# Performance work log

Measured on AMD Instinct MI355X. Metric: run time of the kernel, lower is better.

The kernel has to match this reference:

```python
import jax, jax.numpy as jnp
import numpy as np

B, N, K, H, NF = 4, 4096, 20, 64, 128
EPS = 1e-5  # BatchNorm eps (inference mode)


def _knn_idx(x):
    # x: (B, C, N); returns indices of K nearest neighbors (incl. self), (B, N, K)
    xx = jnp.sum(x * x, axis=1)                      # (B, N)
    inner = jnp.einsum('bcn,bcm->bnm', x, x)         # (B, N, N)
    neg_dist = 2.0 * inner - xx[:, :, None] - xx[:, None, :]
    return jax.lax.top_k(neg_dist, K)[1]


def _graph_feat(x, first):
    # x: (B, C, N) -> edge features (B, C', N, K)
    idx = _knn_idx(x)                                # (B, N, K)
    xt = jnp.transpose(x, (0, 2, 1))                 # (B, N, C)
    nb = jax.vmap(lambda f, i: f[i])(xt, idx)        # (B, N, K, C)
    nb = jnp.transpose(nb, (0, 3, 1, 2))             # (B, C, N, K)
    c = jnp.broadcast_to(x[:, :, :, None], nb.shape)
    parts = [nb - c]
    if first:  # cross term only in first block (3-dim coords)
        parts.append(jnp.cross(c, nb, axis=1))
    parts.append(c)
    return jnp.concatenate(parts, axis=1)


def _conv_bn_lrelu(x, W, g, b, m, v):
    # 1x1 conv (no bias) + BatchNorm (inference) + LeakyReLU(0.2)
    y = jnp.einsum('oc,bc...->bo...', W, x)
    scale = g / jnp.sqrt(v + EPS)
    sh = (1, -1) + (1,) * (y.ndim - 2)
    y = y * scale.reshape(sh) + (b - m * scale).reshape(sh)
    return jnp.where(y >= 0, y, 0.2 * y)


def _forward(x, layers, We, Wh, bh):
    x = jnp.transpose(x, (0, 2, 1))                  # (B, 3, N)
    outs = []
    for li in range(4):
        gf = _graph_feat(x, li == 0)                 # (B, cin, N, K)
        y = _conv_bn_lrelu(gf, *layers[li])          # (B, cout, N, K)
        x = jnp.max(y, axis=-1)                      # max-pool over neighbors
        outs.append(x)
    cat = jnp.concatenate(outs, axis=1)              # (B, 512, N)
    y = _conv_bn_lrelu(cat, *layers[4])              # final Conv1d block
    y = jnp.max(y, axis=-1)                          # global max over points
    emb = y @ We.T                                   # Linear(512, NF, bias=False)
    return emb @ Wh.T + bh                           # embedding_head


def setup_inputs() -> dict:
    key = jax.random.key(0)
    ks = jax.random.split(key, 40)

    def nrm(k, shape, s=0.1):
        return jax.random.normal(k, shape, jnp.float32) * s

    inp = {'x': jax.random.normal(ks[0], (B, N, 3), jnp.float32)}
    dims = [(9, H), (2 * H, H), (2 * H, 2 * H), (4 * H, 4 * H), (8 * H, 8 * H)]
    i = 1
    for li, (cin, cout) in enumerate(dims):
        inp['W%d' % li] = nrm(ks[i], (cout, cin)); i += 1
        inp['g%d' % li] = 1.0 + nrm(ks[i], (cout,), 0.05); i += 1
        inp['b%d' % li] = nrm(ks[i], (cout,), 0.05); i += 1
        inp['m%d' % li] = nrm(ks[i], (cout,), 0.05); i += 1
        inp['v%d' % li] = 1.0 + jax.random.uniform(ks[i], (cout,)) * 0.1; i += 1
    inp['We'] = nrm(ks[i], (NF, 8 * H)); i += 1
    inp['Wh'] = nrm(ks[i], (NF, NF)); i += 1
    inp['bh'] = nrm(ks[i], (NF,))
    return inp


def reference(x, W0, g0, b0, m0, v0, W1, g1, b1, m1, v1, W2, g2, b2, m2, v2,
              W3, g3, b3, m3, v3, W4, g4, b4, m4, v4, We, Wh, bh):
    layers = [(W0, g0, b0, m0, v0), (W1, g1, b1, m1, v1), (W2, g2, b2, m2, v2),
              (W3, g3, b3, m3, v3), (W4, g4, b4, m4, v4)]
    return _forward(x, layers, We, Wh, bh)
```

## Files before the change

### kernel.cpp

```cpp
#include <hip/hip_runtime.h>
#include <cfloat>

#define N_PTS 4096
#define NB    4
#define KNN   20
#define EPSB  1e-5f
#define NSL   4

typedef short s8v __attribute__((ext_vector_type(8)));
typedef float f4v __attribute__((ext_vector_type(4)));

__device__ __forceinline__ void bf16split(float x, unsigned short* h, unsigned short* l)
{
    unsigned u = __builtin_bit_cast(unsigned, x);
    unsigned hb = (u + 0x7fffu + ((u >> 16) & 1u)) >> 16;
    float hf = __builtin_bit_cast(float, hb << 16);
    float res = x - hf;
    unsigned u2 = __builtin_bit_cast(unsigned, res);
    unsigned lb = (u2 + 0x7fffu + ((u2 >> 16) & 1u)) >> 16;
    *h = (unsigned short)hb;
    *l = (unsigned short)lb;
}

__device__ __forceinline__ unsigned packkey(float d, int lc)
{
    d = fmaxf(d, 0.f);
    unsigned u = __builtin_bit_cast(unsigned, d);
    return (u & 0xFFFFFF00u) | (unsigned)lc;
}

__device__ __forceinline__ void insert20k(unsigned key, unsigned (&k20)[KNN])
{
#pragma unroll
    for (int j = 0; j < KNN; j++) {
        unsigned old = k20[j];
        unsigned lo = old < key ? old : key;
        key = old < key ? key : old;
        k20[j] = lo;
    }
}

__device__ __forceinline__ void gl2lds16(const void* g, void* l)
{
    __builtin_amdgcn_global_load_lds(
        (const __attribute__((address_space(1))) unsigned int*)g,
        (__attribute__((address_space(3))) unsigned int*)l,
        16, 0, 0);
}

__device__ __forceinline__ int swz(int g)
{
    return g ^ (((g >> 3) ^ (g >> 6)) & 7);
}

__global__ __launch_bounds__(256)
void to_bf16_pm(const float* __restrict__ F, long bsF, int ldF, int C, int KDP,
                unsigned short* __restrict__ Ghi, unsigned short* __restrict__ Glo)
{
    int b = blockIdx.y;
    int n = blockIdx.x * 64 + (threadIdx.x & 63);
    int kq = threadIdx.x >> 6;
    const float* Fr = F + (long)b * bsF + (long)n * ldF;
    for (int k0 = kq * 8; k0 < KDP; k0 += 32) {
        s8v hv, lv;
#pragma unroll
        for (int i = 0; i < 8; i++) {
            int k = k0 + i;
            float x = (k < C) ? Fr[k] : 0.f;
            unsigned short h, l;
            bf16split(x, &h, &l);
            hv[i] = (short)h;
            lv[i] = (short)l;
        }
        long o = ((long)b * N_PTS + n) * KDP + k0;
        *(s8v*)&Ghi[o] = hv;
        *(s8v*)&Glo[o] = lv;
    }
}

__global__ void sqnorm_pm(const float* __restrict__ F, float* __restrict__ xx,
                          int C, int ldF, long bsF)
{
    int b = blockIdx.y;
    int i = blockIdx.x * 256 + threadIdx.x;
    const float* r = F + (long)b * bsF + (long)i * ldF;
    float s = 0.f;
    for (int c = 0; c < C; c++) s = fmaf(r[c], r[c], s);
    xx[(long)b * N_PTS + i] = s;
}

template<int KDP>
__global__ __launch_bounds__(256, 3)
void fused_knn_mfma7(const unsigned short* __restrict__ Ghi,
                     const unsigned short* __restrict__ Glo,
                     const float* __restrict__ xx,
                     float* __restrict__ knnd, int* __restrict__ knni)
{
    constexpr int KS = KDP / 32;
    constexpr int TS = 16 * KDP;
    constexpr int NCH = (TS * 2) / 16;
    __shared__ short cbuf[2][2][TS];
    __shared__ unsigned mk[4][16][4][KNN];

    int tid = threadIdx.x;
    int w = tid >> 6, L = tid & 63;
    int n = L & 15;
    int quad = L >> 4;
    int b = blockIdx.z, slice = blockIdx.y;
    int q0 = blockIdx.x * 64, qw = w * 16;
    const unsigned short* Gh = Ghi + (long)b * N_PTS * KDP;
    const unsigned short* Gl = Glo + (long)b * N_PTS * KDP;
    const float* xxb = xx + (long)b * N_PTS;

    s8v qhi[KS], qlo[KS];
    long qbase = (long)(q0 + qw + n) * KDP + quad * 8;
#pragma unroll
    for (int ks = 0; ks < KS; ks++) {
        qhi[ks] = *(const s8v*)&Gh[qbase + ks * 32];
        qlo[ks] = *(const s8v*)&Gl[qbase + ks * 32];
    }
    float xq = xxb[q0 + qw + n];

    unsigned k20[KNN];
#pragma unroll
    for (int j = 0; j < KNN; j++) k20[j] = 0xFFFFFFFFu;

    int po[KS];
#pragma unroll
    for (int ks = 0; ks < KS; ks++) {
        int gL = n * (KDP / 8) + quad + ks * 4;
        po[ks] = swz(gL) * 8;
    }
    int gsrc = swz(tid);

    int w64 = tid & 192;
    {
        long tb = (long)(slice * 1024) * KDP;
        if (tid < NCH) {
            gl2lds16((const char*)(Gh + tb) + gsrc * 16,
                     (char*)&cbuf[0][0][0] + w64 * 16);
            gl2lds16((const char*)(Gl + tb) + gsrc * 16,
                     (char*)&cbuf[0][1][0] + w64 * 16);
        }
    }
    __syncthreads();

    const float* xcp = xxb + slice * 1024 + quad * 4;

    for (int t = 0; t < 64; t++) {
        int cur = t & 1;
        if (t < 63 && tid < NCH) {
            long tb = (long)(slice * 1024 + (t + 1) * 16) * KDP;
            gl2lds16((const char*)(Gh + tb) + gsrc * 16,
                     (char*)&cbuf[cur ^ 1][0][0] + w64 * 16);
            gl2lds16((const char*)(Gl + tb) + gsrc * 16,
                     (char*)&cbuf[cur ^ 1][1][0] + w64 * 16);
        }

        const short* Ch = &cbuf[cur][0][0];
        const short* Cl = &cbuf[cur][1][0];
        f4v acc = {0.f, 0.f, 0.f, 0.f};
#pragma unroll
        for (int ks = 0; ks < KS; ks++) {
            s8v chi = *(const s8v*)&Ch[po[ks]];
            s8v clo = *(const s8v*)&Cl[po[ks]];
            acc = __builtin_amdgcn_mfma_f32_16x16x32_bf16(chi, qhi[ks], acc, 0, 0, 0);
            acc = __builtin_amdgcn_mfma_f32_16x16x32_bf16(chi, qlo[ks], acc, 0, 0, 0);
            acc = __builtin_amdgcn_mfma_f32_16x16x32_bf16(clo, qhi[ks], acc, 0, 0, 0);
        }
        float4 xc4 = *(const float4*)xcp;
        float xcv[4] = {xc4.x, xc4.y, xc4.z, xc4.w};
#pragma unroll
        for (int r = 0; r < 4; r++) {
            float d = xq + xcv[r] - 2.f * acc[r];
            insert20k(packkey(d, t * 4 + r), k20);
        }
        xcp += 16;
        __syncthreads();
    }

#pragma unroll
    for (int j = 0; j < KNN; j++) mk[w][n][quad][j] = k20[j];
    __syncthreads();
    if (L < 16) {
        int p[4] = {0, 0, 0, 0};
        long o = (((long)b * NSL + slice) * N_PTS + (q0 + qw + L)) * KNN;
#pragma unroll
        for (int j = 0; j < KNN; j++) {
            unsigned bd = 0xFFFFFF00u; int bi = 0x7fffffff; int bq = 0;
#pragma unroll
            for (int qd = 0; qd < 4; qd++) {
                unsigned kk = mk[w][L][qd][p[qd]];
                unsigned db = kk & 0xFFFFFF00u;
                int lc = (int)(kk & 0xFFu);
                int ci = slice * 1024 + (lc >> 2) * 16 + qd * 4 + (lc & 3);
                if (db < bd || (db == bd && ci < bi)) { bd = db; bi = ci; bq = qd; }
            }
            knnd[o + j] = __builtin_bit_cast(float, bd);
            knni[o + j] = bi;
            p[bq]++;
        }
    }
}

__global__ void knn_merge4(const float* __restrict__ knnd, const int* __restrict__ knni,
                           int* __restrict__ idxOut)
{
    int id = blockIdx.x * 256 + threadIdx.x;
    int b = id / N_PTS, i = id % N_PTS;
    const float* dl[NSL]; const int* il[NSL];
#pragma unroll
    for (int qt = 0; qt < NSL; qt++) {
        dl[qt] = knnd + (((long)b * NSL + qt) * N_PTS + i) * KNN;
        il[qt] = knni + (((long)b * NSL + qt) * N_PTS + i) * KNN;
    }
    int p[NSL];
#pragma unroll
    for (int qt = 0; qt < NSL; qt++) p[qt] = 0;
    int* o = idxOut + (long)id * KNN;
#pragma unroll
    for (int j = 0; j < KNN; j++) {
        float best = FLT_MAX; int bi = 0x7fffffff; int bq = 0;
#pragma unroll
        for (int qt = 0; qt < NSL; qt++) {
            float vv = (p[qt] < KNN) ? dl[qt][p[qt]] : FLT_MAX;
            int   ci = (p[qt] < KNN) ? il[qt][p[qt]] : 0x7fffffff;
            if (vv < best || (vv == best && ci < bi)) { best = vv; bi = ci; bq = qt; }
        }
        o[j] = bi;
        p[bq]++;
    }
}

template<int KDP>
__global__ __launch_bounds__(256)
void qp_mfma(const unsigned short* __restrict__ Ghi,
             const unsigned short* __restrict__ Glo,
             const unsigned short* __restrict__ Wqh, const unsigned short* __restrict__ Wql,
             const unsigned short* __restrict__ Wph, const unsigned short* __restrict__ Wpl,
             const float* __restrict__ shf,
             float* __restrict__ qv, float* __restrict__ pv, int cout)
{
    constexpr int KS = KDP / 32;
    int tid = threadIdx.x;
    int w = tid >> 6, L = tid & 63;
    int n = L & 15, quad = L >> 4;
    int b = blockIdx.z;
    int p0 = blockIdx.x * 64 + w * 16;

    s8v ah[KS], al[KS];
    long abase = ((long)b * N_PTS + p0 + n) * KDP + quad * 8;
#pragma unroll
    for (int ks = 0; ks < KS; ks++) {
        ah[ks] = *(const s8v*)&Ghi[abase + ks * 32];
        al[ks] = *(const s8v*)&Glo[abase + ks * 32];
    }

#pragma unroll
    for (int oc4 = 0; oc4 < 4; oc4++) {
        int oc = blockIdx.y * 4 + oc4;
        long wbase = (long)(oc * 16 + n) * KDP + quad * 8;
        f4v aq = {0.f, 0.f, 0.f, 0.f};
        f4v ap = {0.f, 0.f, 0.f, 0.f};
#pragma unroll
        for (int ks = 0; ks < KS; ks++) {
            s8v wh = *(const s8v*)&Wqh[wbase + ks * 32];
            s8v wl = *(const s8v*)&Wql[wbase + ks * 32];
            aq = __builtin_amdgcn_mfma_f32_16x16x32_bf16(ah[ks], wh, aq, 0, 0, 0);
            aq = __builtin_amdgcn_mfma_f32_16x16x32_bf16(ah[ks], wl, aq, 0, 0, 0);
            aq = __builtin_amdgcn_mfma_f32_16x16x32_bf16(al[ks], wh, aq, 0, 0, 0);
            s8v ph = *(const s8v*)&Wph[wbase + ks * 32];
            s8v pl = *(const s8v*)&Wpl[wbase + ks * 32];
            ap = __builtin_amdgcn_mfma_f32_16x16x32_bf16(ah[ks], ph, ap, 0, 0, 0);
            ap = __builtin_amdgcn_mfma_f32_16x16x32_bf16(ah[ks], pl, ap, 0, 0, 0);
            ap = __builtin_amdgcn_mfma_f32_16x16x32_bf16(al[ks], ph, ap, 0, 0, 0);
        }
        float sv = shf[oc * 16 + n];
#pragma unroll
        for (int r = 0; r < 4; r++) {
            long pt = p0 + quad * 4 + r;
            long o = ((long)b * N_PTS + pt) * cout + oc * 16 + n;
            qv[o] = aq[r];
            pv[o] = ap[r] + sv;
        }
    }
}

__global__ __launch_bounds__(256)
void conv4_mfma(const unsigned short* __restrict__ CTh, const unsigned short* __restrict__ CTl,
                const unsigned short* __restrict__ W4h, const unsigned short* __restrict__ W4l,
                const float* __restrict__ shf, float* __restrict__ Y)
{
    int tid = threadIdx.x;
    int w = tid >> 6, L = tid & 63;
    int n = L & 15, quad = L >> 4;
    int b = blockIdx.y;
    int p0 = blockIdx.x * 16;
    const unsigned short* cth = CTh + ((long)b * N_PTS + p0 + n) * 512 + quad * 8;
    const unsigned short* ctl = CTl + ((long)b * N_PTS + p0 + n) * 512 + quad * 8;

    f4v acc[8];
#pragma unroll
    for (int ch = 0; ch < 8; ch++) acc[ch] = {0.f, 0.f, 0.f, 0.f};

    for (int ks = 0; ks < 16; ks++) {
        s8v bh = *(const s8v*)&cth[ks * 32];
        s8v bl = *(const s8v*)&ctl[ks * 32];
#pragma unroll
        for (int ch = 0; ch < 8; ch++) {
            long o = (long)((w * 8 + ch) * 16 + n) * 512 + quad * 8 + ks * 32;
            s8v ahv = *(const s8v*)&W4h[o];
            s8v alv = *(const s8v*)&W4l[o];
            acc[ch] = __builtin_amdgcn_mfma_f32_16x16x32_bf16(ahv, bh, acc[ch], 0, 0, 0);
            acc[ch] = __builtin_amdgcn_mfma_f32_16x16x32_bf16(ahv, bl, acc[ch], 0, 0, 0);
            acc[ch] = __builtin_amdgcn_mfma_f32_16x16x32_bf16(alv, bh, acc[ch], 0, 0, 0);
        }
    }
#pragma unroll
    for (int ch = 0; ch < 8; ch++) {
#pragma unroll
        for (int r = 0; r < 4; r++) {
            int o = (w * 8 + ch) * 16 + quad * 4 + r;
            float y = acc[ch][r] + shf[o];
            y = y >= 0.f ? y : 0.2f * y;
            Y[((long)b * 512 + o) * N_PTS + p0 + n] = y;
        }
    }
}

__global__ void fold_edge_bf16(const float* __restrict__ W, const float* __restrict__ g,
                               const float* __restrict__ bb, const float* __restrict__ m,
                               const float* __restrict__ v,
                               unsigned short* __restrict__ Wqh, unsigned short* __restrict__ Wql,
                               unsigned short* __restrict__ Wph, unsigned short* __restrict__ Wpl,
                               float* __restrict__ shift, int C, int cout)
{
    int id = blockIdx.x * 256 + threadIdx.x;
    if (id < C * cout) {
        int o = id / C;
        int c = id % C;
        float sc = g[o] * rsqrtf(v[o] + EPSB);
        float wd = W[(long)o * 2 * C + c];
        float wc = W[(long)o * 2 * C + C + c];
        bf16split(sc * wd, &Wqh[id], &Wql[id]);
        bf16split(sc * (wc - wd), &Wph[id], &Wpl[id]);
    }
    if (id < cout) {
        float sc = g[id] * rsqrtf(v[id] + EPSB);
        shift[id] = bb[id] - m[id] * sc;
    }
}

__global__ void fold_plain_bf16(const float* __restrict__ W, const float* __restrict__ g,
                                const float* __restrict__ bb, const float* __restrict__ m,
                                const float* __restrict__ v,
                                unsigned short* __restrict__ W4h, unsigned short* __restrict__ W4l,
                                float* __restrict__ shift, int C, int cout)
{
    int id = blockIdx.x * 256 + threadIdx.x;
    if (id < C * cout) {
        int o = id / C;
        int c = id % C;
        float sc = g[o] * rsqrtf(v[o] + EPSB);
        bf16split(sc * W[(long)o * C + c], &W4h[id], &W4l[id]);
    }
    if (id < cout) {
        float sc = g[id] * rsqrtf(v[id] + EPSB);
        shift[id] = bb[id] - m[id] * sc;
    }
}

__global__ void gather_max_pm(const float* __restrict__ q, const float* __restrict__ p,
                              const int* __restrict__ idx, float* __restrict__ cat,
                              int cout, int c_off)
{
    int b = blockIdx.y;
    int i = blockIdx.x * 4 + threadIdx.y;
    int tx = threadIdx.x;
    const int* ip = idx + ((long)b * N_PTS + i) * KNN;
    int js[KNN];
#pragma unroll
    for (int k = 0; k < KNN; k++) js[k] = ip[k];
    const float* qb = q + (long)b * N_PTS * cout;
    const float* pb = p + ((long)b * N_PTS + i) * cout;
    float* ob = cat + ((long)b * N_PTS + i) * 512 + c_off;
    for (int o0 = 0; o0 < cout; o0 += 64) {
        int o = o0 + tx;
        float pv = pb[o];
        float mx = -FLT_MAX;
#pragma unroll
        for (int k = 0; k < KNN; k++) {
            float val = qb[(long)js[k] * cout + o] + pv;
            val = val >= 0.f ? val : 0.2f * val;
            mx = fmaxf(mx, val);
        }
        ob[o] = mx;
    }
}

__global__ void edge0_pm(const float* __restrict__ x, const int* __restrict__ idx,
                         const float* __restrict__ W0, const float* __restrict__ g0,
                         const float* __restrict__ b0, const float* __restrict__ m0,
                         const float* __restrict__ v0, float* __restrict__ cat)
{
    int b = blockIdx.y;
    int i = blockIdx.x * 4 + threadIdx.y;
    int o = threadIdx.x;
    const float* xc = x + ((long)b * N_PTS + i) * 3;
    float cx = xc[0], cy = xc[1], cz = xc[2];
    float w[9];
#pragma unroll
    for (int c = 0; c < 9; c++) w[c] = W0[o * 9 + c];
    float sc = g0[o] * rsqrtf(v0[o] + EPSB);
    float sh = b0[o] - m0[o] * sc;
    const int* ip = idx + ((long)b * N_PTS + i) * KNN;
    float mx = -FLT_MAX;
#pragma unroll
    for (int k = 0; k < KNN; k++) {
        const float* xn = x + ((long)b * N_PTS + ip[k]) * 3;
        float nx = xn[0], ny = xn[1], nz = xn[2];
        float dx = nx - cx, dy = ny - cy, dz = nz - cz;
        float crx = cy * nz - cz * ny;
        float cry = cz * nx - cx * nz;
        float crz = cx * ny - cy * nx;
        float y = w[0] * dx + w[1] * dy + w[2] * dz
                + w[3] * crx + w[4] * cry + w[5] * crz
                + w[6] * cx + w[7] * cy + w[8] * cz;
        y = y * sc + sh;
        y = y >= 0.f ? y : 0.2f * y;
        mx = fmaxf(mx, y);
    }
    cat[((long)b * N_PTS + i) * 512 + o] = mx;
}

__global__ void rowmax_kernel(const float* __restrict__ Y, float* __restrict__ ymax)
{
    __shared__ float red[256];
    int b = blockIdx.y, o = blockIdx.x, t = threadIdx.x;
    const float* yb = Y + ((long)b * 512 + o) * N_PTS;
    float mx = -FLT_MAX;
#pragma unroll
    for (int s = 0; s < N_PTS / 256; s++) mx = fmaxf(mx, yb[t + 256 * s]);
    red[t] = mx;
    __syncthreads();
    for (int off = 128; off > 0; off >>= 1) {
        if (t < off) red[t] = fmaxf(red[t], red[t + off]);
        __syncthreads();
    }
    if (t == 0) ymax[(long)b * 512 + o] = red[0];
}

__global__ void head_kernel(const float* __restrict__ ymax, const float* __restrict__ We,
                            const float* __restrict__ Wh, const float* __restrict__ bh,
                            float* __restrict__ out)
{
    __shared__ float emb[128];
    __shared__ float yv[512];
    int b = blockIdx.x, t = threadIdx.x;
    for (int s = t; s < 512; s += 128) yv[s] = ymax[(long)b * 512 + s];
    __syncthreads();
    float acc = 0.f;
    for (int c = 0; c < 512; c++) acc = fmaf(yv[c], We[(long)t * 512 + c], acc);
    emb[t] = acc;
    __syncthreads();
    float acc2 = bh[t];
    for (int ff = 0; ff < 128; ff++) acc2 = fmaf(emb[ff], Wh[(long)t * 128 + ff], acc2);
    out[(long)b * 128 + t] = acc2;
}

extern "C" void kernel_launch(void* const* d_in, const int* in_sizes, int n_in,
                              void* d_out, int out_size, void* d_ws, size_t ws_size,
                              hipStream_t stream)
{
    const float* x = (const float*)d_in[0];
    const float *W[5], *g[5], *bb[5], *m[5], *v[5];
    for (int li = 0; li < 5; li++) {
        W[li]  = (const float*)d_in[1 + li * 5 + 0];
        g[li]  = (const float*)d_in[1 + li * 5 + 1];
        bb[li] = (const float*)d_in[1 + li * 5 + 2];
        m[li]  = (const float*)d_in[1 + li * 5 + 3];
        v[li]  = (const float*)d_in[1 + li * 5 + 4];
    }
    const float* We = (const float*)d_in[26];
    const float* Wh = (const float*)d_in[27];
    const float* bh = (const float*)d_in[28];
    float* out = (float*)d_out;

    float* ws   = (float*)d_ws;
    float* cat  = ws;
    float* qbuf = cat + (long)8388608;
    float* pbuf = qbuf + (long)8388608;
    int*   idxb = (int*)(pbuf + 4194304);
    float* xx   = (float*)(idxb + 327680);
    unsigned short* Wqh = (unsigned short*)(xx + 16384);
    unsigned short* Wql = Wqh + 32768;
    unsigned short* Wph = Wql + 32768;
    unsigned short* Wpl = Wph + 32768;
    unsigned short* W4h = Wpl + 32768;
    unsigned short* W4l = W4h + 262144;
    float* shf  = (float*)(W4l + 262144);
    float* ymax = shf + 512;
    unsigned short* Ghi = (unsigned short*)qbuf;
    unsigned short* Glo = Ghi + 2097152;
    float* knnd = qbuf + 2097152;
    int*   knni = (int*)(qbuf + 2097152 + 1310720);
    float* qv   = qbuf + 2097152;
    unsigned short* CTh = (unsigned short*)qbuf;
    unsigned short* CTl = CTh + 8388608;

    sqnorm_pm<<<dim3(16, NB), dim3(256), 0, stream>>>(x, xx, 3, 3, (long)3 * N_PTS);
    to_bf16_pm<<<dim3(64, NB), dim3(256), 0, stream>>>(
        x, (long)3 * N_PTS, 3, 3, 32, Ghi, Glo);
    fused_knn_mfma7<32><<<dim3(64, NSL, NB), dim3(256), 0, stream>>>(
        Ghi, Glo, xx, knnd, knni);
    knn_merge4<<<dim3(64), dim3(256), 0, stream>>>(knnd, knni, idxb);
    edge0_pm<<<dim3(N_PTS / 4, NB), dim3(64, 4), 0, stream>>>(
        x, idxb, W[0], g[0], bb[0], m[0], v[0], cat);

    const int Cs_[3]   = {64, 64, 128};
    const int co_[3]   = {64, 128, 256};
    const int inO_[3]  = {0, 64, 128};
    const int outO_[3] = {64, 128, 256};
    for (int s = 0; s < 3; s++) {
        int C = Cs_[s], cout = co_[s];
        const float* F = cat + inO_[s];
        sqnorm_pm<<<dim3(16, NB), dim3(256), 0, stream>>>(
            F, xx, C, 512, (long)N_PTS * 512);
        to_bf16_pm<<<dim3(64, NB), dim3(256), 0, stream>>>(
            F, (long)N_PTS * 512, 512, C, C, Ghi, Glo);
        if (C == 64)
            fused_knn_mfma7<64><<<dim3(64, NSL, NB), dim3(256), 0, stream>>>(
                Ghi, Glo, xx, knnd, knni);
        else
            fused_knn_mfma7<128><<<dim3(64, NSL, NB), dim3(256), 0, stream>>>(
                Ghi, Glo, xx, knnd, knni);
        knn_merge4<<<dim3(64), dim3(256), 0, stream>>>(knnd, knni, idxb);

        int li = s + 1;
        fold_edge_bf16<<<dim3((C * cout + 255) / 256), dim3(256), 0, stream>>>(
            W[li], g[li], bb[li], m[li], v[li], Wqh, Wql, Wph, Wpl, shf, C, cout);
        if (C == 64)
            qp_mfma<64><<<dim3(64, cout / 64, NB), dim3(256), 0, stream>>>(
                Ghi, Glo, Wqh, Wql, Wph, Wpl, shf, qv, pbuf, cout);
        else
            qp_mfma<128><<<dim3(64, cout / 64, NB), dim3(256), 0, stream>>>(
                Ghi, Glo, Wqh, Wql, Wph, Wpl, shf, qv, pbuf, cout);
        gather_max_pm<<<dim3(N_PTS / 4, NB), dim3(64, 4), 0, stream>>>(
            qv, pbuf, idxb, cat, cout, outO_[s]);
    }

    fold_plain_bf16<<<dim3((512 * 512 + 255) / 256), dim3(256), 0, stream>>>(
        W[4], g[4], bb[4], m[4], v[4], W4h, W4l, shf, 512, 512);
    to_bf16_pm<<<dim3(64, NB), dim3(256), 0, stream>>>(
        cat, (long)N_PTS * 512, 512, 512, 512, CTh, CTl);
    conv4_mfma<<<dim3(N_PTS / 16, NB), dim3(256), 0, stream>>>(
        CTh, CTl, W4h, W4l, shf, cat);

    rowmax_kernel<<<dim3(512, NB), dim3(256), 0, stream>>>(cat, ymax);
    head_kernel<<<dim3(NB), dim3(128), 0, stream>>>(ymax, We, Wh, bh, out);
}
```

Baseline: 1.097 ms.

## Fuse bf16 split and squared norms into producer kernels, drop standalone conversion passes

The edge0 and gather-max kernels now emit the bf16 hi/lo split and per-point squared norm of their output directly, replacing the separate sqnorm and to_bf16 passes before each kNN stage. The final conv reads fp32 cat and splits to bf16 in-register, removing the 512-channel conversion pass and its buffer. Conv output goes to a separate buffer instead of overwriting cat. This trades extra conversion ALU work inside conv4 (repeated per block) for fewer launches and less memory traffic.

```diff
diff --git a/kernel.cpp b/kernel.cpp
--- a/kernel.cpp
+++ b/kernel.cpp
@@ -287,25 +287,33 @@
 }
 
 __global__ __launch_bounds__(256)
-void conv4_mfma(const unsigned short* __restrict__ CTh, const unsigned short* __restrict__ CTl,
-                const unsigned short* __restrict__ W4h, const unsigned short* __restrict__ W4l,
-                const float* __restrict__ shf, float* __restrict__ Y)
+void conv4f_mfma(const float* __restrict__ cat,
+                 const unsigned short* __restrict__ W4h, const unsigned short* __restrict__ W4l,
+                 const float* __restrict__ shf, float* __restrict__ Y)
 {
     int tid = threadIdx.x;
     int w = tid >> 6, L = tid & 63;
     int n = L & 15, quad = L >> 4;
     int b = blockIdx.y;
     int p0 = blockIdx.x * 16;
-    const unsigned short* cth = CTh + ((long)b * N_PTS + p0 + n) * 512 + quad * 8;
-    const unsigned short* ctl = CTl + ((long)b * N_PTS + p0 + n) * 512 + quad * 8;
+    const float* cr = cat + ((long)b * N_PTS + p0 + n) * 512 + quad * 8;
 
     f4v acc[8];
 #pragma unroll
     for (int ch = 0; ch < 8; ch++) acc[ch] = {0.f, 0.f, 0.f, 0.f};
 
     for (int ks = 0; ks < 16; ks++) {
-        s8v bh = *(const s8v*)&cth[ks * 32];
-        s8v bl = *(const s8v*)&ctl[ks * 32];
+        float4 f0 = *(const float4*)&cr[ks * 32];
+        float4 f1 = *(const float4*)&cr[ks * 32 + 4];
+        float fv[8] = {f0.x, f0.y, f0.z, f0.w, f1.x, f1.y, f1.z, f1.w};
+        s8v bh, bl;
+#pragma unroll
+        for (int i = 0; i < 8; i++) {
+            unsigned short h, l;
+            bf16split(fv[i], &h, &l);
+            bh[i] = (short)h;
+            bl[i] = (short)l;
+        }
 #pragma unroll
         for (int ch = 0; ch < 8; ch++) {
             long o = (long)((w * 8 + ch) * 16 + n) * 512 + quad * 8 + ks * 32;
@@ -370,9 +378,12 @@
     }
 }
 
-__global__ void gather_max_pm(const float* __restrict__ q, const float* __restrict__ p,
-                              const int* __restrict__ idx, float* __restrict__ cat,
-                              int cout, int c_off)
+__global__ void gather_max_fused(const float* __restrict__ q, const float* __restrict__ p,
+                                 const int* __restrict__ idx, float* __restrict__ cat,
+                                 int cout, int c_off,
+                                 unsigned short* __restrict__ Ghi,
+                                 unsigned short* __restrict__ Glo,
+                                 float* __restrict__ xx)
 {
     int b = blockIdx.y;
     int i = blockIdx.x * 4 + threadIdx.y;
@@ -384,6 +395,7 @@
     const float* qb = q + (long)b * N_PTS * cout;
     const float* pb = p + ((long)b * N_PTS + i) * cout;
     float* ob = cat + ((long)b * N_PTS + i) * 512 + c_off;
+    float ssum = 0.f;
     for (int o0 = 0; o0 < cout; o0 += 64) {
         int o = o0 + tx;
         float pv = pb[o];
@@ -395,13 +407,29 @@
             mx = fmaxf(mx, val);
         }
         ob[o] = mx;
-    }
-}
-
-__global__ void edge0_pm(const float* __restrict__ x, const int* __restrict__ idx,
-                         const float* __restrict__ W0, const float* __restrict__ g0,
-                         const float* __restrict__ b0, const float* __restrict__ m0,
-                         const float* __restrict__ v0, float* __restrict__ cat)
+        if (Ghi) {
+            unsigned short h, l;
+            bf16split(mx, &h, &l);
+            long go = ((long)b * N_PTS + i) * cout + o;
+            Ghi[go] = h;
+            Glo[go] = l;
+            ssum = fmaf(mx, mx, ssum);
+        }
+    }
+    if (Ghi) {
+#pragma unroll
+        for (int off = 32; off > 0; off >>= 1) ssum += __shfl_xor(ssum, off);
+        if (tx == 0) xx[(long)b * N_PTS + i] = ssum;
+    }
+}
+
+__global__ void edge0_fused(const float* __restrict__ x, const int* __restrict__ idx,
+                            const float* __restrict__ W0, const float* __restrict__ g0,
+                            const float* __restrict__ b0, const float* __restrict__ m0,
+                            const float* __restrict__ v0, float* __restrict__ cat,
+                            unsigned short* __restrict__ Ghi,
+                            unsigned short* __restrict__ Glo,
+                            float* __restrict__ xx)
 {
     int b = blockIdx.y;
     int i = blockIdx.x * 4 + threadIdx.y;
@@ -431,6 +459,15 @@
         mx = fmaxf(mx, y);
     }
     cat[((long)b * N_PTS + i) * 512 + o] = mx;
+    unsigned short h, l;
+    bf16split(mx, &h, &l);
+    long go = ((long)b * N_PTS + i) * 64 + o;
+    Ghi[go] = h;
+    Glo[go] = l;
+    float ssum = mx * mx;
+#pragma unroll
+    for (int off = 32; off > 0; off >>= 1) ssum += __shfl_xor(ssum, off);
+    if (o == 0) xx[(long)b * N_PTS + i] = ssum;
 }
 
 __global__ void rowmax_kernel(const float* __restrict__ Y, float* __restrict__ ymax)
@@ -505,8 +542,7 @@
     float* knnd = qbuf + 2097152;
     int*   knni = (int*)(qbuf + 2097152 + 1310720);
     float* qv   = qbuf + 2097152;
-    unsigned short* CTh = (unsigned short*)qbuf;
-    unsigned short* CTl = CTh + 8388608;
+    float* Ybuf = qbuf;
 
     sqnorm_pm<<<dim3(16, NB), dim3(256), 0, stream>>>(x, xx, 3, 3, (long)3 * N_PTS);
     to_bf16_pm<<<dim3(64, NB), dim3(256), 0, stream>>>(
@@ -514,20 +550,14 @@
     fused_knn_mfma7<32><<<dim3(64, NSL, NB), dim3(256), 0, stream>>>(
         Ghi, Glo, xx, knnd, knni);
     knn_merge4<<<dim3(64), dim3(256), 0, stream>>>(knnd, knni, idxb);
-    edge0_pm<<<dim3(N_PTS / 4, NB), dim3(64, 4), 0, stream>>>(
-        x, idxb, W[0], g[0], bb[0], m[0], v[0], cat);
+    edge0_fused<<<dim3(N_PTS / 4, NB), dim3(64, 4), 0, stream>>>(
+        x, idxb, W[0], g[0], bb[0], m[0], v[0], cat, Ghi, Glo, xx);
 
     const int Cs_[3]   = {64, 64, 128};
     const int co_[3]   = {64, 128, 256};
-    const int inO_[3]  = {0, 64, 128};
     const int outO_[3] = {64, 128, 256};
     for (int s = 0; s < 3; s++) {
         int C = Cs_[s], cout = co_[s];
-        const float* F = cat + inO_[s];
-        sqnorm_pm<<<dim3(16, NB), dim3(256), 0, stream>>>(
-            F, xx, C, 512, (long)N_PTS * 512);
-        to_bf16_pm<<<dim3(64, NB), dim3(256), 0, stream>>>(
-            F, (long)N_PTS * 512, 512, C, C, Ghi, Glo);
         if (C == 64)
             fused_knn_mfma7<64><<<dim3(64, NSL, NB), dim3(256), 0, stream>>>(
                 Ghi, Glo, xx, knnd, knni);
@@ -545,17 +575,20 @@
         else
             qp_mfma<128><<<dim3(64, cout / 64, NB), dim3(256), 0, stream>>>(
                 Ghi, Glo, Wqh, Wql, Wph, Wpl, shf, qv, pbuf, cout);
-        gather_max_pm<<<dim3(N_PTS / 4, NB), dim3(64, 4), 0, stream>>>(
-            qv, pbuf, idxb, cat, cout, outO_[s]);
+        if (s < 2)
+            gather_max_fused<<<dim3(N_PTS / 4, NB), dim3(64, 4), 0, stream>>>(
+                qv, pbuf, idxb, cat, cout, outO_[s], Ghi, Glo, xx);
+        else
+            gather_max_fused<<<dim3(N_PTS / 4, NB), dim3(64, 4), 0, stream>>>(
+                qv, pbuf, idxb, cat, cout, outO_[s],
+                (unsigned short*)nullptr, (unsigned short*)nullptr, (float*)nullptr);
     }
 
     fold_plain_bf16<<<dim3((512 * 512 + 255) / 256), dim3(256), 0, stream>>>(
         W[4], g[4], bb[4], m[4], v[4], W4h, W4l, shf, 512, 512);
-    to_bf16_pm<<<dim3(64, NB), dim3(256), 0, stream>>>(
-        cat, (long)N_PTS * 512, 512, 512, 512, CTh, CTl);
-    conv4_mfma<<<dim3(N_PTS / 16, NB), dim3(256), 0, stream>>>(
-        CTh, CTl, W4h, W4l, shf, cat);
-
-    rowmax_kernel<<<dim3(512, NB), dim3(256), 0, stream>>>(cat, ymax);
+    conv4f_mfma<<<dim3(N_PTS / 16, NB), dim3(256), 0, stream>>>(
+        cat, W4h, W4l, shf, Ybuf);
+
+    rowmax_kernel<<<dim3(512, NB), dim3(256), 0, stream>>>(Ybuf, ymax);
     head_kernel<<<dim3(NB), dim3(128), 0, stream>>>(ymax, We, Wh, bh, out);
 }
```

Result: faster. 1.062 ms (-3.2%).
